# Optimization experiments

Hardware: AMD Instinct MI355X
Metric: run time of the kernel (lower is better)

## Reference

```python
import jax, jax.numpy as jnp
import numpy as np

B, T, C, H = 4, 2048, 768, 12
D = C // H  # head_size = 64
ROPE_BASE = 10000.0


def rotary_tables(seq_len, dim, dtype=jnp.float32):
    # dim = head_size; uses dim//2 frequencies
    inv_freq = 1.0 / (ROPE_BASE ** (jnp.arange(0, dim, 2, dtype=jnp.float32) / dim))
    t = jnp.arange(seq_len, dtype=jnp.float32)
    freqs = jnp.outer(t, inv_freq)  # [T, D/2]
    return jnp.cos(freqs).astype(dtype), jnp.sin(freqs).astype(dtype)


def apply_rotary(x, cos, sin):
    # x: [B, H, T, D]; cos/sin: [T, D/2] broadcast over B,H
    d = x.shape[-1] // 2
    x1, x2 = x[..., :d], x[..., d:]
    y1 = x1 * cos + x2 * sin
    y2 = -x1 * sin + x2 * cos
    return jnp.concatenate([y1, y2], axis=-1)


def setup_inputs() -> dict:
    key = jax.random.key(0)
    ks = jax.random.split(key, 5)
    x = jax.random.normal(ks[0], (B, T, C), dtype=jnp.float32)
    W_attn = jax.random.normal(ks[1], (C, 3 * C), dtype=jnp.float32) * (1.0 / np.sqrt(C))
    b_attn = jax.random.normal(ks[2], (3 * C,), dtype=jnp.float32) * 0.02
    W_proj = jax.random.normal(ks[3], (C, C), dtype=jnp.float32) * (1.0 / np.sqrt(C))
    b_proj = jax.random.normal(ks[4], (C,), dtype=jnp.float32) * 0.02
    return {"x": x, "W_attn": W_attn, "b_attn": b_attn, "W_proj": W_proj, "b_proj": b_proj}


def reference(x, W_attn, b_attn, W_proj, b_proj):
    Bx, Tx, Cx = x.shape
    qkv = x @ W_attn + b_attn  # [B, T, 3C]
    q, k, v = jnp.split(qkv, 3, axis=-1)
    # [B, T, C] -> [B, H, T, D]
    to_heads = lambda a: a.reshape(Bx, Tx, H, D).transpose(0, 2, 1, 3)
    q, k, v = to_heads(q), to_heads(k), to_heads(v)
    cos, sin = rotary_tables(Tx, D, x.dtype)
    q = apply_rotary(q, cos, sin)
    k = apply_rotary(k, cos, sin)
    scale = 1.0 / np.sqrt(D)
    scores = jnp.einsum('bhqd,bhkd->bhqk', q, k) * scale  # [B, H, T, T]
    causal = jnp.tril(jnp.ones((Tx, Tx), dtype=bool))
    scores = jnp.where(causal, scores, jnp.finfo(scores.dtype).min)
    attn = jax.nn.softmax(scores, axis=-1)
    y = jnp.einsum('bhqk,bhkd->bhqd', attn, v)  # [B, H, T, D]
    y = y.transpose(0, 2, 1, 3).reshape(Bx, Tx, Cx)
    return y @ W_proj + b_proj
```

## Files before the change

### kernel.cpp

```cpp
#include <hip/hip_runtime.h>
#include <hip/hip_bf16.h>

#define BB 4
#define TT 2048
#define CC 768
#define HH 12
#define DD 64
#define MM (BB * TT)
#define BH (BB * HH)

typedef __bf16 bf16_t;
typedef __bf16 bf16x8 __attribute__((ext_vector_type(8)));
typedef __bf16 bf16x4 __attribute__((ext_vector_type(4)));
typedef float f32x4 __attribute__((ext_vector_type(4)));

__device__ __forceinline__ float fast_exp2(float x) {
#if __has_builtin(__builtin_amdgcn_exp2f)
    return __builtin_amdgcn_exp2f(x);
#else
    return exp2f(x);
#endif
}

__device__ __forceinline__ uint32_t pk2(float lo, float hi) {
    bf16_t l = (bf16_t)lo, h = (bf16_t)hi;
    uint16_t lu = __builtin_bit_cast(uint16_t, l);
    uint16_t hu = __builtin_bit_cast(uint16_t, h);
    return ((uint32_t)hu << 16) | lu;
}

__device__ __forceinline__ void gload_lds16(const void* g, void* l) {
    __builtin_amdgcn_global_load_lds(
        (const __attribute__((address_space(1))) uint32_t*)g,
        (__attribute__((address_space(3))) uint32_t*)l, 16, 0, 0);
}

__global__ void cvt_f32_bf16(const float* __restrict__ in, bf16_t* __restrict__ out, int n4) {
    int tid = blockIdx.x * blockDim.x + threadIdx.x;
    if (tid >= n4) return;
    float4 v = ((const float4*)in)[tid];
    bf16x4 o;
    o[0] = (bf16_t)v.x; o[1] = (bf16_t)v.y; o[2] = (bf16_t)v.z; o[3] = (bf16_t)v.w;
    ((bf16x4*)out)[tid] = o;
}

__global__ void transpose_cvt(const float* __restrict__ W, bf16_t* __restrict__ WT, int K, int N) {
    __shared__ bf16_t tile[32][33];
    int k0 = blockIdx.x * 32, n0 = blockIdx.y * 32;
    int tx = threadIdx.x, ty = threadIdx.y;
#pragma unroll
    for (int r = 0; r < 4; ++r) {
        int kl = ty * 4 + r;
        tile[kl][tx] = (bf16_t)W[(size_t)(k0 + kl) * N + n0 + tx];
    }
    __syncthreads();
#pragma unroll
    for (int r = 0; r < 4; ++r) {
        int nl = ty * 4 + r;
        WT[(size_t)(n0 + nl) * K + k0 + tx] = tile[tx][nl];
    }
}

#define GEMM_CORE(A_, BT_, acc_)                                                       \
    __shared__ bf16_t As[2][128 * 32];                                                 \
    __shared__ bf16_t Bs[2][128 * 32];                                                 \
    int tid = threadIdx.x;                                                             \
    int wv = tid >> 6, lane = tid & 63, c = lane & 15, quad = lane >> 4;               \
    int wm = (wv >> 1) * 64, wn = (wv & 1) * 64;                                       \
    int m0 = blockIdx.x * 128, n0 = blockIdx.y * 128;                                  \
    int srow = wv * 32 + (lane >> 2);                                                  \
    int slot = lane & 3;                                                               \
    auto stage = [&](int buf, int k0) {                                                \
        _Pragma("unroll")                                                              \
        for (int ins = 0; ins < 2; ++ins) {                                            \
            int r = srow + ins * 16;                                                   \
            int g = (slot - ((r >> 1) & 3)) & 3;                                       \
            const bf16_t* ga = A_ + (size_t)(m0 + r) * K + k0 + g * 8;                 \
            const bf16_t* gb = BT_ + (size_t)(n0 + r) * K + k0 + g * 8;                \
            gload_lds16(ga, &As[buf][(wv * 32 + ins * 16) * 32]);                      \
            gload_lds16(gb, &Bs[buf][(wv * 32 + ins * 16) * 32]);                      \
        }                                                                              \
    };                                                                                 \
    int s_rd = (quad + ((c >> 1) & 3)) & 3;                                            \
    const int nk = K / 32;                                                             \
    stage(0, 0);                                                                       \
    for (int kt = 0; kt < nk; ++kt) {                                                  \
        __syncthreads();                                                               \
        if (kt + 1 < nk) stage((kt + 1) & 1, (kt + 1) * 32);                           \
        int buf = kt & 1;                                                              \
        bf16x8 af[4], bfr[4];                                                          \
        _Pragma("unroll")                                                              \
        for (int i = 0; i < 4; ++i) af[i] = *(const bf16x8*)&As[buf][(wm + i * 16 + c) * 32 + s_rd * 8];  \
        _Pragma("unroll")                                                              \
        for (int j = 0; j < 4; ++j) bfr[j] = *(const bf16x8*)&Bs[buf][(wn + j * 16 + c) * 32 + s_rd * 8]; \
        _Pragma("unroll")                                                              \
        for (int i = 0; i < 4; ++i)                                                    \
            _Pragma("unroll")                                                          \
            for (int j = 0; j < 4; ++j)                                                \
                acc_[i][j] = __builtin_amdgcn_mfma_f32_16x16x32_bf16(af[i], bfr[j], acc_[i][j], 0, 0, 0); \
    }

__global__ __launch_bounds__(256, 3) void gemm_qkv(
        const bf16_t* __restrict__ A, const bf16_t* __restrict__ BT,
        const float* __restrict__ bias,
        bf16_t* __restrict__ Qh, bf16_t* __restrict__ Kh, bf16_t* __restrict__ Vt) {
    const int K = 768;
    __shared__ __align__(16) bf16_t smem[17408];
    bf16_t* Asp = smem;
    bf16_t* Bsp = smem + 8192;
    int tid = threadIdx.x;
    int wv = tid >> 6, lane = tid & 63, c = lane & 15, quad = lane >> 4;
    int wm = (wv >> 1) * 64, wn = (wv & 1) * 64;
    int m0 = blockIdx.x * 128, n0 = blockIdx.y * 128;
    int srow = wv * 32 + (lane >> 2);
    int slot = lane & 3;
    auto stage = [&](int buf, int k0) {
#pragma unroll
        for (int ins = 0; ins < 2; ++ins) {
            int r = srow + ins * 16;
            int g = (slot - ((r >> 1) & 3)) & 3;
            gload_lds16(A + (size_t)(m0 + r) * K + k0 + g * 8, &Asp[buf * 4096 + (wv * 32 + ins * 16) * 32]);
            gload_lds16(BT + (size_t)(n0 + r) * K + k0 + g * 8, &Bsp[buf * 4096 + (wv * 32 + ins * 16) * 32]);
        }
    };
    int s_rd = (quad + ((c >> 1) & 3)) & 3;
    f32x4 acc[4][4] = {};
    const int nk = K / 32;
    stage(0, 0);
    for (int kt = 0; kt < nk; ++kt) {
        __syncthreads();
        if (kt + 1 < nk) stage((kt + 1) & 1, (kt + 1) * 32);
        int buf = kt & 1;
        bf16x8 af[4], bfr[4];
#pragma unroll
        for (int i = 0; i < 4; ++i) af[i] = *(const bf16x8*)&Asp[buf * 4096 + (wm + i * 16 + c) * 32 + s_rd * 8];
#pragma unroll
        for (int j = 0; j < 4; ++j) bfr[j] = *(const bf16x8*)&Bsp[buf * 4096 + (wn + j * 16 + c) * 32 + s_rd * 8];
#pragma unroll
        for (int i = 0; i < 4; ++i)
#pragma unroll
            for (int j = 0; j < 4; ++j)
                acc[i][j] = __builtin_amdgcn_mfma_f32_16x16x32_bf16(af[i], bfr[j], acc[i][j], 0, 0, 0);
    }
    __syncthreads();

    int type = n0 / 768;
    int hloc = ((n0 % 768) + wn) >> 6;
    int bidx = m0 >> 11;
    int colb = n0 + wn;
    int tb = (m0 + wm) & (TT - 1);
    bf16_t* epi = smem + wv * 4352;
    int rrow = lane >> 3, cchunk = lane & 7;

    if (type < 2) {
        const float rscale = (type == 0) ? 0.125f * 1.44269504088896f : 1.0f;
#pragma unroll
        for (int j = 0; j < 2; ++j) {
            int dlo = j * 16 + c;
            float infr = fast_exp2(-(float)dlo * 0.4152410118609828f);
            float blo = bias[colb + j * 16 + c];
            float bhi = bias[colb + (j + 2) * 16 + c];
#pragma unroll
            for (int i = 0; i < 4; ++i)
#pragma unroll
                for (int r = 0; r < 4; ++r) {
                    int lr = i * 16 + quad * 4 + r;
                    float a = acc[i][j][r] + blo;
                    float b2 = acc[i][j + 2][r] + bhi;
                    float fr = (float)(tb + lr) * infr;
                    float cs, sn;
                    __sincosf(fr, &sn, &cs);
                    epi[lr * 68 + dlo]      = (bf16_t)((a * cs + b2 * sn) * rscale);
                    epi[lr * 68 + dlo + 32] = (bf16_t)((-a * sn + b2 * cs) * rscale);
                }
        }
        bf16_t* dst = (type == 0 ? Qh : Kh) + (size_t)(bidx * HH + hloc) * TT * DD + (size_t)tb * DD;
#pragma unroll
        for (int it = 0; it < 8; ++it) {
            int row = it * 8 + rrow;
            bf16x8 v = *(const bf16x8*)&epi[row * 68 + cchunk * 8];
            *(bf16x8*)&dst[row * 64 + cchunk * 8] = v;
        }
    } else {
        int kt64 = tb >> 6;
#pragma unroll
        for (int j = 0; j < 4; ++j) {
            int dim = j * 16 + c;
            float bv = bias[colb + j * 16 + c];
            int rot = (dim & 7) * 8;
#pragma unroll
            for (int i = 0; i < 4; ++i)
#pragma unroll
                for (int r = 0; r < 4; ++r) {
                    int tin = i * 16 + quad * 4 + r;
                    epi[dim * 68 + ((tin + rot) & 63)] = (bf16_t)(acc[i][j][r] + bv);
                }
        }
        bf16_t* dstV = Vt + (size_t)(bidx * HH + hloc) * (TT / 64) * 4096 + (size_t)kt64 * 4096;
#pragma unroll
        for (int it = 0; it < 8; ++it) {
            int dim = it * 8 + rrow;
            int src = ((cchunk + (dim & 7)) & 7) * 8;
            bf16x8 v = *(const bf16x8*)&epi[dim * 68 + src];
            *(bf16x8*)&dstV[dim * 64 + cchunk * 8] = v;
        }
    }
}

__global__ __launch_bounds__(256, 3) void gemm_proj(
        const bf16_t* __restrict__ A, const bf16_t* __restrict__ BT,
        const float* __restrict__ bias, float* __restrict__ Cout) {
    const int K = 768;
    f32x4 acc[4][4] = {};
    GEMM_CORE(A, BT, acc)
#pragma unroll
    for (int j = 0; j < 4; ++j) {
        int col = n0 + wn + j * 16 + c;
        float bv = bias[col];
#pragma unroll
        for (int i = 0; i < 4; ++i) {
            int row = m0 + wm + i * 16 + quad * 4;
#pragma unroll
            for (int r = 0; r < 4; ++r)
                Cout[(size_t)(row + r) * CC + col] = acc[i][j][r] + bv;
        }
    }
}

__global__ __launch_bounds__(256, 3) void flash_attn(
        const bf16_t* __restrict__ Q, const bf16_t* __restrict__ Kc,
        const bf16_t* __restrict__ Vt, bf16_t* __restrict__ Y) {
    __shared__ bf16_t Ks[2][64 * 64];
    __shared__ bf16_t Vs[2][64 * 64];
    int blk = blockIdx.x;
    int qt = 15 - blk / BH;
    int bh = blk % BH;
    int wv = threadIdx.x >> 6, lane = threadIdx.x & 63;
    int b = bh / HH, h = bh - b * HH;
    int c = lane & 15, quad = lane >> 4;
    int qbw = qt * 128 + wv * 32;
    const bf16_t* Qg = Q + ((size_t)bh * TT + qbw) * DD;
    const bf16_t* Kg = Kc + (size_t)bh * TT * DD;
    const bf16_t* Vg = Vt + (size_t)bh * (TT / 64) * 4096;

    bf16x8 qf[2][2];
#pragma unroll
    for (int s = 0; s < 2; ++s)
#pragma unroll
        for (int ch = 0; ch < 2; ++ch)
            qf[s][ch] = *(const bf16x8*)(Qg + (s * 16 + c) * DD + ch * 32 + quad * 8);

    int srow = wv * 16 + (lane >> 3);
    int slot = lane & 7;
    auto stage = [&](int buf, int kt64) {
#pragma unroll
        for (int ins = 0; ins < 2; ++ins) {
            int r = srow + ins * 8;
            int g = (slot - (r & 7)) & 7;
            gload_lds16(Kg + (size_t)(kt64 * 64 + r) * 64 + g * 8, &Ks[buf][(wv * 16 + ins * 8) * 64]);
            gload_lds16(Vg + (size_t)kt64 * 4096 + r * 64 + g * 8, &Vs[buf][(wv * 16 + ins * 8) * 64]);
        }
    };

    f32x4 O[2][4] = {};
    float lsum[2] = {0.0f, 0.0f};
    int lane_lo = c + ((quad & 1) << 5);
    int lane_hi = lane_lo + 16;
    bool lowq = (quad < 2);

    int ntiles = 2 * qt + 2;
    stage(0, 0);
    for (int kt = 0; kt < ntiles; ++kt) {
        __syncthreads();
        if (kt + 1 < ntiles) stage((kt + 1) & 1, kt + 1);
        int buf = kt & 1;
#pragma unroll
        for (int t32 = 0; t32 < 2; ++t32) {
            int ks = kt * 64 + t32 * 32;
            if (ks > qbw) continue;
            bool masked = (ks == qbw);
            bf16x8 kf[2][2], vf[4];
#pragma unroll
            for (int t2 = 0; t2 < 2; ++t2)
#pragma unroll
                for (int ch = 0; ch < 2; ++ch) {
                    int row = t32 * 32 + t2 * 16 + c;
                    int sl = (ch * 4 + quad + (c & 7)) & 7;
                    kf[t2][ch] = *(const bf16x8*)&Ks[buf][row * 64 + sl * 8];
                }
#pragma unroll
            for (int nt = 0; nt < 4; ++nt) {
                int row = nt * 16 + c;
                int sl = (t32 * 4 + quad + (c & 7)) & 7;
                vf[nt] = *(const bf16x8*)&Vs[buf][row * 64 + sl * 8];
            }
            f32x4 st[2][2] = {};
#pragma unroll
            for (int s = 0; s < 2; ++s)
#pragma unroll
                for (int t2 = 0; t2 < 2; ++t2) {
                    st[s][t2] = __builtin_amdgcn_mfma_f32_16x16x32_bf16(kf[t2][0], qf[s][0], st[s][t2], 0, 0, 0);
                    st[s][t2] = __builtin_amdgcn_mfma_f32_16x16x32_bf16(kf[t2][1], qf[s][1], st[s][t2], 0, 0, 0);
                }
#pragma unroll
            for (int s = 0; s < 2; ++s) {
                float pv[2][4];
#pragma unroll
                for (int t2 = 0; t2 < 2; ++t2)
#pragma unroll
                    for (int r = 0; r < 4; ++r) {
                        float p = fast_exp2(st[s][t2][r]);
                        if (masked) {
                            int keyl = t2 * 16 + quad * 4 + r;
                            if (keyl > s * 16 + c) p = 0.0f;
                        }
                        pv[t2][r] = p;
                    }
                lsum[s] += ((pv[0][0] + pv[0][1]) + (pv[0][2] + pv[0][3]))
                         + ((pv[1][0] + pv[1][1]) + (pv[1][2] + pv[1][3]));
                uint32_t pk0a = pk2(pv[0][0], pv[0][1]), pk0b = pk2(pv[0][2], pv[0][3]);
                uint32_t pk1a = pk2(pv[1][0], pv[1][1]), pk1b = pk2(pv[1][2], pv[1][3]);
                union { uint32_t u[4]; bf16x8 v; } pf;
                {
                    uint32_t x0 = (uint32_t)__shfl((int)pk0a, lane_lo);
                    uint32_t y0 = (uint32_t)__shfl((int)pk1a, lane_lo);
                    pf.u[0] = lowq ? x0 : y0;
                    uint32_t x1 = (uint32_t)__shfl((int)pk0b, lane_lo);
                    uint32_t y1 = (uint32_t)__shfl((int)pk1b, lane_lo);
                    pf.u[1] = lowq ? x1 : y1;
                    uint32_t x2 = (uint32_t)__shfl((int)pk0a, lane_hi);
                    uint32_t y2 = (uint32_t)__shfl((int)pk1a, lane_hi);
                    pf.u[2] = lowq ? x2 : y2;
                    uint32_t x3 = (uint32_t)__shfl((int)pk0b, lane_hi);
                    uint32_t y3 = (uint32_t)__shfl((int)pk1b, lane_hi);
                    pf.u[3] = lowq ? x3 : y3;
                }
#pragma unroll
                for (int nt = 0; nt < 4; ++nt)
                    O[s][nt] = __builtin_amdgcn_mfma_f32_16x16x32_bf16(vf[nt], pf.v, O[s][nt], 0, 0, 0);
            }
        }
    }

#pragma unroll
    for (int s = 0; s < 2; ++s) {
        float l = lsum[s];
        l += __shfl_xor(l, 16);
        l += __shfl_xor(l, 32);
        float inv_l = 1.0f / l;
        int row = b * TT + qbw + s * 16 + c;
#pragma unroll
        for (int nt = 0; nt < 4; ++nt) {
            bf16x4 ov;
#pragma unroll
            for (int r = 0; r < 4; ++r) ov[r] = (bf16_t)(O[s][nt][r] * inv_l);
            *(bf16x4*)(Y + (size_t)row * CC + h * DD + nt * 16 + quad * 4) = ov;
        }
    }
}

extern "C" void kernel_launch(void* const* d_in, const int* in_sizes, int n_in,
                              void* d_out, int out_size, void* d_ws, size_t ws_size,
                              hipStream_t stream) {
    const float* x      = (const float*)d_in[0];
    const float* W_attn = (const float*)d_in[1];
    const float* b_attn = (const float*)d_in[2];
    const float* W_proj = (const float*)d_in[3];
    const float* b_proj = (const float*)d_in[4];
    float* out = (float*)d_out;

    unsigned char* ws = (unsigned char*)d_ws;
    size_t off = 0;
    auto alloc = [&](size_t bytes) { void* p = ws + off; off += (bytes + 255) & ~(size_t)255; return p; };
    bf16_t* xb  = (bf16_t*)alloc((size_t)MM * CC * 2);
    bf16_t* WaT = (bf16_t*)alloc((size_t)3 * CC * CC * 2);
    bf16_t* WpT = (bf16_t*)alloc((size_t)CC * CC * 2);
    bf16_t* Qh  = (bf16_t*)alloc((size_t)BH * TT * DD * 2);
    bf16_t* Kh  = (bf16_t*)alloc((size_t)BH * TT * DD * 2);
    bf16_t* Vt  = (bf16_t*)alloc((size_t)BH * TT * DD * 2);
    bf16_t* Yb  = (bf16_t*)alloc((size_t)MM * CC * 2);

    cvt_f32_bf16<<<(MM * CC / 4 + 255) / 256, 256, 0, stream>>>(x, xb, MM * CC / 4);
    transpose_cvt<<<dim3(CC / 32, 3 * CC / 32), dim3(32, 8), 0, stream>>>(W_attn, WaT, CC, 3 * CC);
    transpose_cvt<<<dim3(CC / 32, CC / 32), dim3(32, 8), 0, stream>>>(W_proj, WpT, CC, CC);
    gemm_qkv<<<dim3(MM / 128, 3 * CC / 128), 256, 0, stream>>>(xb, WaT, b_attn, Qh, Kh, Vt);
    flash_attn<<<dim3(768), 256, 0, stream>>>(Qh, Kh, Vt, Yb);
    gemm_proj<<<dim3(MM / 128, CC / 128), 256, 0, stream>>>(Yb, WpT, b_proj, out);
}
```

Before: 200.4 us.

## Remap GEMM blocks per XCD and balance causal attention work by pairing query tiles

The two GEMMs move to a 1D grid whose block index is remapped so that consecutive blocks on the same XCD share M-tiles, aiming for better L2 reuse of A/B tiles. Flash attention drops to 128-thread blocks that each handle two 64-row query tiles (tq and 31-tq). This pairing balances the causal triangle so every block does equal work. Heads are grouped by XCD to keep K/V in the local L2. The cost is that each block loops its two phases one after the other, with fewer waves per block and more global staging per wave.

```diff
diff --git a/kernel.cpp b/kernel.cpp
--- a/kernel.cpp
+++ b/kernel.cpp
@@ -61,13 +61,15 @@
     }
 }
 
-#define GEMM_CORE(A_, BT_, acc_)                                                       \
+#define GEMM_CORE(A_, BT_, acc_, NY_)                                                  \
     __shared__ bf16_t As[2][128 * 32];                                                 \
     __shared__ bf16_t Bs[2][128 * 32];                                                 \
     int tid = threadIdx.x;                                                             \
     int wv = tid >> 6, lane = tid & 63, c = lane & 15, quad = lane >> 4;               \
     int wm = (wv >> 1) * 64, wn = (wv & 1) * 64;                                       \
-    int m0 = blockIdx.x * 128, n0 = blockIdx.y * 128;                                  \
+    int bid = blockIdx.x;                                                              \
+    int m0 = ((bid & 7) + 8 * (bid / (8 * NY_))) * 128;                                \
+    int n0 = ((bid >> 3) % NY_) * 128;                                                 \
     int srow = wv * 32 + (lane >> 2);                                                  \
     int slot = lane & 3;                                                               \
     auto stage = [&](int buf, int k0) {                                                \
@@ -105,13 +107,16 @@
         const float* __restrict__ bias,
         bf16_t* __restrict__ Qh, bf16_t* __restrict__ Kh, bf16_t* __restrict__ Vt) {
     const int K = 768;
+    const int NY = 18;
     __shared__ __align__(16) bf16_t smem[17408];
     bf16_t* Asp = smem;
     bf16_t* Bsp = smem + 8192;
     int tid = threadIdx.x;
     int wv = tid >> 6, lane = tid & 63, c = lane & 15, quad = lane >> 4;
     int wm = (wv >> 1) * 64, wn = (wv & 1) * 64;
-    int m0 = blockIdx.x * 128, n0 = blockIdx.y * 128;
+    int bid = blockIdx.x;
+    int m0 = ((bid & 7) + 8 * (bid / (8 * NY))) * 128;
+    int n0 = ((bid >> 3) % NY) * 128;
     int srow = wv * 32 + (lane >> 2);
     int slot = lane & 3;
     auto stage = [&](int buf, int k0) {
@@ -212,7 +217,7 @@
         const float* __restrict__ bias, float* __restrict__ Cout) {
     const int K = 768;
     f32x4 acc[4][4] = {};
-    GEMM_CORE(A, BT, acc)
+    GEMM_CORE(A, BT, acc, 6)
 #pragma unroll
     for (int j = 0; j < 4; ++j) {
         int col = n0 + wn + j * 16 + c;
@@ -227,135 +232,144 @@
     }
 }
 
-__global__ __launch_bounds__(256, 3) void flash_attn(
+__global__ __launch_bounds__(128, 2) void flash_attn(
         const bf16_t* __restrict__ Q, const bf16_t* __restrict__ Kc,
         const bf16_t* __restrict__ Vt, bf16_t* __restrict__ Y) {
     __shared__ bf16_t Ks[2][64 * 64];
     __shared__ bf16_t Vs[2][64 * 64];
     int blk = blockIdx.x;
-    int qt = 15 - blk / BH;
-    int bh = blk % BH;
+    int xcd = blk & 7;
+    int rest = blk >> 3;
+    int bh = xcd * 6 + rest % 6;
+    int a = rest / 6;
     int wv = threadIdx.x >> 6, lane = threadIdx.x & 63;
     int b = bh / HH, h = bh - b * HH;
     int c = lane & 15, quad = lane >> 4;
-    int qbw = qt * 128 + wv * 32;
-    const bf16_t* Qg = Q + ((size_t)bh * TT + qbw) * DD;
     const bf16_t* Kg = Kc + (size_t)bh * TT * DD;
     const bf16_t* Vg = Vt + (size_t)bh * (TT / 64) * 4096;
 
-    bf16x8 qf[2][2];
-#pragma unroll
-    for (int s = 0; s < 2; ++s)
-#pragma unroll
-        for (int ch = 0; ch < 2; ++ch)
-            qf[s][ch] = *(const bf16x8*)(Qg + (s * 16 + c) * DD + ch * 32 + quad * 8);
-
-    int srow = wv * 16 + (lane >> 3);
+    int srow8 = lane >> 3;
     int slot = lane & 7;
     auto stage = [&](int buf, int kt64) {
 #pragma unroll
-        for (int ins = 0; ins < 2; ++ins) {
-            int r = srow + ins * 8;
+        for (int ins = 0; ins < 4; ++ins) {
+            int r = wv * 32 + ins * 8 + srow8;
             int g = (slot - (r & 7)) & 7;
-            gload_lds16(Kg + (size_t)(kt64 * 64 + r) * 64 + g * 8, &Ks[buf][(wv * 16 + ins * 8) * 64]);
-            gload_lds16(Vg + (size_t)kt64 * 4096 + r * 64 + g * 8, &Vs[buf][(wv * 16 + ins * 8) * 64]);
+            gload_lds16(Kg + (size_t)(kt64 * 64 + r) * 64 + g * 8, &Ks[buf][(wv * 32 + ins * 8) * 64]);
+            gload_lds16(Vg + (size_t)kt64 * 4096 + r * 64 + g * 8, &Vs[buf][(wv * 32 + ins * 8) * 64]);
         }
     };
 
-    f32x4 O[2][4] = {};
-    float lsum[2] = {0.0f, 0.0f};
     int lane_lo = c + ((quad & 1) << 5);
     int lane_hi = lane_lo + 16;
     bool lowq = (quad < 2);
 
-    int ntiles = 2 * qt + 2;
-    stage(0, 0);
-    for (int kt = 0; kt < ntiles; ++kt) {
+#pragma unroll
+    for (int ph = 0; ph < 2; ++ph) {
+        int tq = (ph == 0) ? (31 - a) : a;
+        int qbw = tq * 64 + wv * 32;
+        const bf16_t* Qg = Q + ((size_t)bh * TT + qbw) * DD;
+
+        bf16x8 qf[2][2];
+#pragma unroll
+        for (int s = 0; s < 2; ++s)
+#pragma unroll
+            for (int ch = 0; ch < 2; ++ch)
+                qf[s][ch] = *(const bf16x8*)(Qg + (s * 16 + c) * DD + ch * 32 + quad * 8);
+
+        f32x4 O[2][4] = {};
+        float lsum[2] = {0.0f, 0.0f};
+
+        int ntiles = tq + 1;
+        stage(0, 0);
+        for (int kt = 0; kt < ntiles; ++kt) {
+            __syncthreads();
+            if (kt + 1 < ntiles) stage((kt + 1) & 1, kt + 1);
+            int buf = kt & 1;
+#pragma unroll
+            for (int t32 = 0; t32 < 2; ++t32) {
+                int ks = kt * 64 + t32 * 32;
+                if (ks > qbw) continue;
+                bool masked = (ks == qbw);
+                bf16x8 kf[2][2], vf[4];
+#pragma unroll
+                for (int t2 = 0; t2 < 2; ++t2)
+#pragma unroll
+                    for (int ch = 0; ch < 2; ++ch) {
+                        int row = t32 * 32 + t2 * 16 + c;
+                        int sl = (ch * 4 + quad + (c & 7)) & 7;
+                        kf[t2][ch] = *(const bf16x8*)&Ks[buf][row * 64 + sl * 8];
+                    }
+#pragma unroll
+                for (int nt = 0; nt < 4; ++nt) {
+                    int row = nt * 16 + c;
+                    int sl = (t32 * 4 + quad + (c & 7)) & 7;
+                    vf[nt] = *(const bf16x8*)&Vs[buf][row * 64 + sl * 8];
+                }
+                f32x4 st[2][2] = {};
+#pragma unroll
+                for (int s = 0; s < 2; ++s)
+#pragma unroll
+                    for (int t2 = 0; t2 < 2; ++t2) {
+                        st[s][t2] = __builtin_amdgcn_mfma_f32_16x16x32_bf16(kf[t2][0], qf[s][0], st[s][t2], 0, 0, 0);
+                        st[s][t2] = __builtin_amdgcn_mfma_f32_16x16x32_bf16(kf[t2][1], qf[s][1], st[s][t2], 0, 0, 0);
+                    }
+#pragma unroll
+                for (int s = 0; s < 2; ++s) {
+                    float pv[2][4];
+#pragma unroll
+                    for (int t2 = 0; t2 < 2; ++t2)
+#pragma unroll
+                        for (int r = 0; r < 4; ++r) {
+                            float p = fast_exp2(st[s][t2][r]);
+                            if (masked) {
+                                int keyl = t2 * 16 + quad * 4 + r;
+                                if (keyl > s * 16 + c) p = 0.0f;
+                            }
+                            pv[t2][r] = p;
+                        }
+                    lsum[s] += ((pv[0][0] + pv[0][1]) + (pv[0][2] + pv[0][3]))
+                             + ((pv[1][0] + pv[1][1]) + (pv[1][2] + pv[1][3]));
+                    uint32_t pk0a = pk2(pv[0][0], pv[0][1]), pk0b = pk2(pv[0][2], pv[0][3]);
+                    uint32_t pk1a = pk2(pv[1][0], pv[1][1]), pk1b = pk2(pv[1][2], pv[1][3]);
+                    union { uint32_t u[4]; bf16x8 v; } pf;
+                    {
+                        uint32_t x0 = (uint32_t)__shfl((int)pk0a, lane_lo);
+                        uint32_t y0 = (uint32_t)__shfl((int)pk1a, lane_lo);
+                        pf.u[0] = lowq ? x0 : y0;
+                        uint32_t x1 = (uint32_t)__shfl((int)pk0b, lane_lo);
+                        uint32_t y1 = (uint32_t)__shfl((int)pk1b, lane_lo);
+                        pf.u[1] = lowq ? x1 : y1;
+                        uint32_t x2 = (uint32_t)__shfl((int)pk0a, lane_hi);
+                        uint32_t y2 = (uint32_t)__shfl((int)pk1a, lane_hi);
+                        pf.u[2] = lowq ? x2 : y2;
+                        uint32_t x3 = (uint32_t)__shfl((int)pk0b, lane_hi);
+                        uint32_t y3 = (uint32_t)__shfl((int)pk1b, lane_hi);
+                        pf.u[3] = lowq ? x3 : y3;
+                    }
+#pragma unroll
+                    for (int nt = 0; nt < 4; ++nt)
+                        O[s][nt] = __builtin_amdgcn_mfma_f32_16x16x32_bf16(vf[nt], pf.v, O[s][nt], 0, 0, 0);
+                }
+            }
+        }
+
+#pragma unroll
+        for (int s = 0; s < 2; ++s) {
+            float l = lsum[s];
+            l += __shfl_xor(l, 16);
+            l += __shfl_xor(l, 32);
+            float inv_l = 1.0f / l;
+            int row = b * TT + qbw + s * 16 + c;
+#pragma unroll
+            for (int nt = 0; nt < 4; ++nt) {
+                bf16x4 ov;
+#pragma unroll
+                for (int r = 0; r < 4; ++r) ov[r] = (bf16_t)(O[s][nt][r] * inv_l);
+                *(bf16x4*)(Y + (size_t)row * CC + h * DD + nt * 16 + quad * 4) = ov;
+            }
+        }
         __syncthreads();
-        if (kt + 1 < ntiles) stage((kt + 1) & 1, kt + 1);
-        int buf = kt & 1;
-#pragma unroll
-        for (int t32 = 0; t32 < 2; ++t32) {
-            int ks = kt * 64 + t32 * 32;
-            if (ks > qbw) continue;
-            bool masked = (ks == qbw);
-            bf16x8 kf[2][2], vf[4];
-#pragma unroll
-            for (int t2 = 0; t2 < 2; ++t2)
-#pragma unroll
-                for (int ch = 0; ch < 2; ++ch) {
-                    int row = t32 * 32 + t2 * 16 + c;
-                    int sl = (ch * 4 + quad + (c & 7)) & 7;
-                    kf[t2][ch] = *(const bf16x8*)&Ks[buf][row * 64 + sl * 8];
-                }
-#pragma unroll
-            for (int nt = 0; nt < 4; ++nt) {
-                int row = nt * 16 + c;
-                int sl = (t32 * 4 + quad + (c & 7)) & 7;
-                vf[nt] = *(const bf16x8*)&Vs[buf][row * 64 + sl * 8];
-            }
-            f32x4 st[2][2] = {};
-#pragma unroll
-            for (int s = 0; s < 2; ++s)
-#pragma unroll
-                for (int t2 = 0; t2 < 2; ++t2) {
-                    st[s][t2] = __builtin_amdgcn_mfma_f32_16x16x32_bf16(kf[t2][0], qf[s][0], st[s][t2], 0, 0, 0);
-                    st[s][t2] = __builtin_amdgcn_mfma_f32_16x16x32_bf16(kf[t2][1], qf[s][1], st[s][t2], 0, 0, 0);
-                }
-#pragma unroll
-            for (int s = 0; s < 2; ++s) {
-                float pv[2][4];
-#pragma unroll
-                for (int t2 = 0; t2 < 2; ++t2)
-#pragma unroll
-                    for (int r = 0; r < 4; ++r) {
-                        float p = fast_exp2(st[s][t2][r]);
-                        if (masked) {
-                            int keyl = t2 * 16 + quad * 4 + r;
-                            if (keyl > s * 16 + c) p = 0.0f;
-                        }
-                        pv[t2][r] = p;
-                    }
-                lsum[s] += ((pv[0][0] + pv[0][1]) + (pv[0][2] + pv[0][3]))
-                         + ((pv[1][0] + pv[1][1]) + (pv[1][2] + pv[1][3]));
-                uint32_t pk0a = pk2(pv[0][0], pv[0][1]), pk0b = pk2(pv[0][2], pv[0][3]);
-                uint32_t pk1a = pk2(pv[1][0], pv[1][1]), pk1b = pk2(pv[1][2], pv[1][3]);
-                union { uint32_t u[4]; bf16x8 v; } pf;
-                {
-                    uint32_t x0 = (uint32_t)__shfl((int)pk0a, lane_lo);
-                    uint32_t y0 = (uint32_t)__shfl((int)pk1a, lane_lo);
-                    pf.u[0] = lowq ? x0 : y0;
-                    uint32_t x1 = (uint32_t)__shfl((int)pk0b, lane_lo);
-                    uint32_t y1 = (uint32_t)__shfl((int)pk1b, lane_lo);
-                    pf.u[1] = lowq ? x1 : y1;
-                    uint32_t x2 = (uint32_t)__shfl((int)pk0a, lane_hi);
-                    uint32_t y2 = (uint32_t)__shfl((int)pk1a, lane_hi);
-                    pf.u[2] = lowq ? x2 : y2;
-                    uint32_t x3 = (uint32_t)__shfl((int)pk0b, lane_hi);
-                    uint32_t y3 = (uint32_t)__shfl((int)pk1b, lane_hi);
-                    pf.u[3] = lowq ? x3 : y3;
-                }
-#pragma unroll
-                for (int nt = 0; nt < 4; ++nt)
-                    O[s][nt] = __builtin_amdgcn_mfma_f32_16x16x32_bf16(vf[nt], pf.v, O[s][nt], 0, 0, 0);
-            }
-        }
-    }
-
-#pragma unroll
-    for (int s = 0; s < 2; ++s) {
-        float l = lsum[s];
-        l += __shfl_xor(l, 16);
-        l += __shfl_xor(l, 32);
-        float inv_l = 1.0f / l;
-        int row = b * TT + qbw + s * 16 + c;
-#pragma unroll
-        for (int nt = 0; nt < 4; ++nt) {
-            bf16x4 ov;
-#pragma unroll
-            for (int r = 0; r < 4; ++r) ov[r] = (bf16_t)(O[s][nt][r] * inv_l);
-            *(bf16x4*)(Y + (size_t)row * CC + h * DD + nt * 16 + quad * 4) = ov;
-        }
     }
 }
 
@@ -383,7 +397,7 @@
     cvt_f32_bf16<<<(MM * CC / 4 + 255) / 256, 256, 0, stream>>>(x, xb, MM * CC / 4);
     transpose_cvt<<<dim3(CC / 32, 3 * CC / 32), dim3(32, 8), 0, stream>>>(W_attn, WaT, CC, 3 * CC);
     transpose_cvt<<<dim3(CC / 32, CC / 32), dim3(32, 8), 0, stream>>>(W_proj, WpT, CC, CC);
-    gemm_qkv<<<dim3(MM / 128, 3 * CC / 128), 256, 0, stream>>>(xb, WaT, b_attn, Qh, Kh, Vt);
-    flash_attn<<<dim3(768), 256, 0, stream>>>(Qh, Kh, Vt, Yb);
-    gemm_proj<<<dim3(MM / 128, CC / 128), 256, 0, stream>>>(Yb, WpT, b_proj, out);
-}
+    gemm_qkv<<<dim3(64 * 18), 256, 0, stream>>>(xb, WaT, b_attn, Qh, Kh, Vt);
+    flash_attn<<<dim3(768), 128, 0, stream>>>(Qh, Kh, Vt, Yb);
+    gemm_proj<<<dim3(64 * 6), 256, 0, stream>>>(Yb, WpT, b_proj, out);
+}
```

After: 224.1 us. 1.12x slower.
